# Kernel tuning notes

Measured on AMD Instinct MI355X. Metric: run time of the kernel, lower is better.

## Reference

```python
import jax, jax.numpy as jnp
import numpy as np

N_NODES = 50000
N_EDGES = 1600000
IN_FEATS = 32
HIDDEN = 64
OUT_FEAT = 64


def setup_inputs() -> dict:
    key = jax.random.key(0)
    ks = jax.random.split(key, 8)
    inputs = jax.random.normal(ks[0], (N_NODES, IN_FEATS), dtype=jnp.float32)
    edge_weights = jax.random.uniform(ks[1], (N_EDGES, 1), dtype=jnp.float32)
    src = jax.random.randint(ks[2], (N_EDGES,), 0, N_NODES, dtype=jnp.int32)
    dst = jax.random.randint(ks[3], (N_EDGES,), 0, N_NODES, dtype=jnp.int32)
    W1 = jax.random.normal(ks[4], (IN_FEATS, HIDDEN), dtype=jnp.float32) / np.sqrt(IN_FEATS)
    b1 = jnp.zeros((HIDDEN,), dtype=jnp.float32)
    W2 = jax.random.normal(ks[5], (HIDDEN + IN_FEATS, OUT_FEAT), dtype=jnp.float32) / np.sqrt(HIDDEN + IN_FEATS)
    b2 = jnp.zeros((OUT_FEAT,), dtype=jnp.float32)
    return {"inputs": inputs, "edge_weights": edge_weights, "src": src, "dst": dst,
            "W1": W1, "b1": b1, "W2": W2, "b2": b2}


def _weighted_graph_conv(x, W, b, src, dst, ew, src_norm, dst_norm, n_nodes):
    # x: [N, Din] -> [N, Dout]
    x = x @ W                               # dense projection
    x = x * src_norm                        # D_out^{-1/2} scaling at source
    m = x[src] * ew                         # [E, Dout] gather * edge weight
    h = jax.ops.segment_sum(m, dst, num_segments=n_nodes)  # scatter-sum at dest
    return h * dst_norm + b                 # D_in^{-1/2} scaling + bias


def reference(inputs, edge_weights, src, dst, W1, b1, W2, b2):
    n = inputs.shape[0]
    ones = jnp.ones((src.shape[0],), dtype=jnp.float32)
    out_deg = jax.ops.segment_sum(ones, src, num_segments=n)
    in_deg = jax.ops.segment_sum(ones, dst, num_segments=n)
    src_norm = jnp.clip(out_deg, 1.0, None)[:, None] ** -0.5  # [N,1]
    dst_norm = jnp.clip(in_deg, 1.0, None)[:, None] ** -0.5   # [N,1]

    h = _weighted_graph_conv(inputs, W1, b1, src, dst, edge_weights, src_norm, dst_norm, n)
    h = jax.nn.relu(h)
    reminder = jnp.concatenate([h, inputs], axis=-1)  # re-inject input features
    h = _weighted_graph_conv(reminder, W2, b2, src, dst, edge_weights, src_norm, dst_norm, n)
    h = jax.nn.relu(h)
    # torch F.normalize(p=2, dim=-1, eps=1e-12)
    norm = jnp.linalg.norm(h, axis=-1, keepdims=True)
    return h / jnp.maximum(norm, 1e-12)
```

## Files before the change

### kernel.cpp

```cpp
#include <hip/hip_runtime.h>
#include <math.h>


#define BUK 128
#define BUK_SHIFT 7
#define FSH 256
#define SS 128
#define HIST_BS 512
#define NBUK_MAX 512
#define MAX_LDS_BYTES 131072
#define PROJ_GRID 512

#define SCAN_BS 256
#define SCAN_ITEMS 4
#define SCAN_CHUNK (SCAN_BS * SCAN_ITEMS)

__device__ __forceinline__ unsigned short f2bf(float f) {
    unsigned u = __float_as_uint(f);
    return (unsigned short)((u + 0x7fffu + ((u >> 16) & 1u)) >> 16);
}
__device__ __forceinline__ float bf2f(unsigned short h) {
    return __uint_as_float((unsigned)h << 16);
}
__device__ __forceinline__ float rlane(float v, int k) {
    return __uint_as_float(__builtin_amdgcn_readlane(__float_as_uint(v), k));
}

__device__ __forceinline__ float edge_gather(const int* __restrict__ offsets,
                                             const unsigned* __restrict__ edata,
                                             const unsigned short* __restrict__ xp,
                                             int n, int lane) {
    int beg = offsets[n];
    int end = offsets[n + 1];
    float a0 = 0.f, a1 = 0.f, a2 = 0.f, a3 = 0.f;
    for (int p = beg; p < end; p += 64) {
        int cnt = min(64, end - p);
        unsigned eb = (p + lane < end) ? edata[p + lane] : 0u;
        int k = 0;
        for (; k + 7 < cnt; k += 8) {
            unsigned e0 = __builtin_amdgcn_readlane(eb, k);
            unsigned e1 = __builtin_amdgcn_readlane(eb, k + 1);
            unsigned e2 = __builtin_amdgcn_readlane(eb, k + 2);
            unsigned e3 = __builtin_amdgcn_readlane(eb, k + 3);
            unsigned e4 = __builtin_amdgcn_readlane(eb, k + 4);
            unsigned e5 = __builtin_amdgcn_readlane(eb, k + 5);
            unsigned e6 = __builtin_amdgcn_readlane(eb, k + 6);
            unsigned e7 = __builtin_amdgcn_readlane(eb, k + 7);
            float v0 = bf2f(xp[(size_t)(e0 & 0xffffu) * 64 + lane]);
            float v1 = bf2f(xp[(size_t)(e1 & 0xffffu) * 64 + lane]);
            float v2 = bf2f(xp[(size_t)(e2 & 0xffffu) * 64 + lane]);
            float v3 = bf2f(xp[(size_t)(e3 & 0xffffu) * 64 + lane]);
            float v4 = bf2f(xp[(size_t)(e4 & 0xffffu) * 64 + lane]);
            float v5 = bf2f(xp[(size_t)(e5 & 0xffffu) * 64 + lane]);
            float v6 = bf2f(xp[(size_t)(e6 & 0xffffu) * 64 + lane]);
            float v7 = bf2f(xp[(size_t)(e7 & 0xffffu) * 64 + lane]);
            a0 = fmaf(v0, bf2f((unsigned short)(e0 >> 16)), a0);
            a1 = fmaf(v1, bf2f((unsigned short)(e1 >> 16)), a1);
            a2 = fmaf(v2, bf2f((unsigned short)(e2 >> 16)), a2);
            a3 = fmaf(v3, bf2f((unsigned short)(e3 >> 16)), a3);
            a0 = fmaf(v4, bf2f((unsigned short)(e4 >> 16)), a0);
            a1 = fmaf(v5, bf2f((unsigned short)(e5 >> 16)), a1);
            a2 = fmaf(v6, bf2f((unsigned short)(e6 >> 16)), a2);
            a3 = fmaf(v7, bf2f((unsigned short)(e7 >> 16)), a3);
        }
        for (; k < cnt; ++k) {
            unsigned e0 = __builtin_amdgcn_readlane(eb, k);
            a0 = fmaf(bf2f(xp[(size_t)(e0 & 0xffffu) * 64 + lane]),
                      bf2f((unsigned short)(e0 >> 16)), a0);
        }
    }
    return (a0 + a1) + (a2 + a3);
}

__global__ void hist_src_kernel(const int* __restrict__ src, unsigned* __restrict__ partial_s,
                                int E, int NW4, int sliceS) {
    extern __shared__ unsigned h[];
    for (int i = threadIdx.x; i < NW4; i += blockDim.x) h[i] = 0u;
    __syncthreads();
    int s = blockIdx.x;
    int beg = s * sliceS, end = min(beg + sliceS, E);
    for (int e = beg + (int)threadIdx.x; e < end; e += blockDim.x) {
        int v = src[e];
        atomicAdd(&h[v >> 2], 1u << (8 * (v & 3)));
    }
    __syncthreads();
    unsigned* o = partial_s + (size_t)s * NW4;
    for (int i = threadIdx.x; i < NW4; i += blockDim.x) o[i] = h[i];
}

__global__ void reduce_src_kernel(const unsigned* __restrict__ partial_s,
                                  float* __restrict__ srcn, int N, int NW4) {
    int w = blockIdx.x * blockDim.x + threadIdx.x;
    if (w >= NW4) return;
    unsigned run = 0;
#pragma unroll 4
    for (int s = 0; s < SS; ++s) run += partial_s[(size_t)s * NW4 + w];
    int n0 = 4 * w;
#pragma unroll
    for (int k = 0; k < 4; ++k) {
        int n = n0 + k;
        if (n < N) srcn[n] = rsqrtf(fmaxf((float)((run >> (8 * k)) & 0xffu), 1.0f));
    }
}

__global__ void count_kernel(const int* __restrict__ dst, int* __restrict__ cntmat,
                             int E, int L, int NBUK) {
    __shared__ int c[NBUK_MAX];
    for (int i = threadIdx.x; i < NBUK; i += blockDim.x) c[i] = 0;
    __syncthreads();
    int s = blockIdx.x;
    int beg = s * L, end = min(beg + L, E);
    for (int e = beg + (int)threadIdx.x; e < end; e += blockDim.x)
        atomicAdd(&c[dst[e] >> BUK_SHIFT], 1);
    __syncthreads();
    for (int b = threadIdx.x; b < NBUK; b += blockDim.x)
        cntmat[(size_t)b * FSH + s] = c[b];
}

__global__ void scan_partial(const int* __restrict__ deg, int* __restrict__ bsum, int N) {
    __shared__ int sdata[SCAN_BS];
    int t = threadIdx.x;
    int base = blockIdx.x * SCAN_CHUNK + t * SCAN_ITEMS;
    int s = 0;
#pragma unroll
    for (int k = 0; k < SCAN_ITEMS; ++k) {
        int idx = base + k;
        s += (idx < N) ? deg[idx] : 0;
    }
    sdata[t] = s;
    __syncthreads();
    for (int off = SCAN_BS / 2; off > 0; off >>= 1) {
        if (t < off) sdata[t] += sdata[t + off];
        __syncthreads();
    }
    if (t == 0) bsum[blockIdx.x] = sdata[0];
}

__global__ void scan_bsums(int* __restrict__ bsum, int NB) {
    int carry = 0;
    for (int base = 0; base < NB; base += 64) {
        int l = base + (int)threadIdx.x;
        int v = (l < NB) ? bsum[l] : 0;
        int inc = v;
#pragma unroll
        for (int off = 1; off < 64; off <<= 1) {
            int tv = __shfl_up(inc, off, 64);
            if ((int)threadIdx.x >= off) inc += tv;
        }
        if (l < NB) bsum[l] = carry + inc - v;
        carry += __shfl(inc, 63, 64);
    }
}

__global__ void scan_final(const int* __restrict__ deg, const int* __restrict__ bsum,
                           int* __restrict__ offsets, int N) {
    __shared__ int sdata[SCAN_BS];
    int t = threadIdx.x;
    int base = blockIdx.x * SCAN_CHUNK + t * SCAN_ITEMS;
    int loc[SCAN_ITEMS];
    int s = 0;
#pragma unroll
    for (int k = 0; k < SCAN_ITEMS; ++k) {
        int idx = base + k;
        loc[k] = (idx < N) ? deg[idx] : 0;
        s += loc[k];
    }
    sdata[t] = s;
    __syncthreads();
    for (int off = 1; off < SCAN_BS; off <<= 1) {
        int v = (t >= off) ? sdata[t - off] : 0;
        __syncthreads();
        sdata[t] += v;
        __syncthreads();
    }
    int excl = sdata[t] - s + bsum[blockIdx.x];
#pragma unroll
    for (int k = 0; k < SCAN_ITEMS; ++k) {
        int idx = base + k;
        if (idx < N) {
            offsets[idx] = excl;
            if (idx == N - 1) offsets[N] = excl + loc[k];
        }
        excl += loc[k];
    }
}

__global__ void place_seg_kernel(const int* __restrict__ src, const int* __restrict__ dst,
                                 const float* __restrict__ ew, const int* __restrict__ cscan,
                                 uint2* __restrict__ inter, int E, int L, int NBUK) {
    __shared__ int cur[NBUK_MAX];
    int s = blockIdx.x;
    for (int b = threadIdx.x; b < NBUK; b += blockDim.x)
        cur[b] = cscan[(size_t)b * FSH + s];
    __syncthreads();
    int beg = s * L, end = min(beg + L, E);
    for (int e = beg + (int)threadIdx.x; e < end; e += blockDim.x) {
        int d = dst[e];
        int b = d >> BUK_SHIFT;
        int pos = atomicAdd(&cur[b], 1);
        inter[pos] = make_uint2((unsigned)src[e] | ((unsigned)f2bf(ew[e]) << 16),
                                (unsigned)(d & (BUK - 1)));
    }
}

__global__ void fill_final_kernel(const uint2* __restrict__ inter,
                                  const int* __restrict__ cscan,
                                  unsigned* __restrict__ edata, int* __restrict__ offsets,
                                  float* __restrict__ dstn, int N, int NBUK) {
    __shared__ int cnt[BUK];
    __shared__ int loff[BUK];
    int b = blockIdx.x;
    int t = threadIdx.x;
    int beg = cscan[(size_t)b * FSH];
    int end = cscan[(size_t)(b + 1) * FSH];
    if (t < BUK) cnt[t] = 0;
    __syncthreads();
    for (int p = beg + t; p < end; p += blockDim.x)
        atomicAdd(&cnt[inter[p].y], 1);
    __syncthreads();
    if (t < 64) {
        int carry = 0;
#pragma unroll
        for (int base = 0; base < BUK; base += 64) {
            int v = cnt[base + t];
            int inc = v;
#pragma unroll
            for (int off = 1; off < 64; off <<= 1) {
                int tv = __shfl_up(inc, off, 64);
                if (t >= off) inc += tv;
            }
            loff[base + t] = carry + inc - v;
            carry += __shfl(inc, 63, 64);
        }
    }
    __syncthreads();
    int node0 = b << BUK_SHIFT;
    if (t < BUK) {
        int n = node0 + t;
        if (n < N) {
            offsets[n] = beg + loff[t];
            dstn[n] = rsqrtf(fmaxf((float)cnt[t], 1.0f));
        }
    }
    if (b == NBUK - 1 && t == 0) offsets[N] = end;
    __syncthreads();
    if (t < BUK) cnt[t] = 0;
    __syncthreads();
    for (int p = beg + t; p < end; p += blockDim.x) {
        uint2 r = inter[p];
        int dl = (int)r.y;
        int rk = atomicAdd(&cnt[dl], 1);
        edata[beg + loff[dl] + rk] = r.x;
    }
}

__global__ void proj1_kernel(const float* __restrict__ X, const float* __restrict__ W1,
                             const float* __restrict__ srcn,
                             unsigned short* __restrict__ xp, int N) {
    __shared__ float w[32 * 64];
    int tid = threadIdx.x;
    {
        const float4* Wv = (const float4*)W1;
        float4* wv = (float4*)w;
        for (int i = tid; i < 512; i += 256) wv[i] = Wv[i];
    }
    __syncthreads();
    int lane = tid & 63;
    int wid = tid >> 6;
    int half = lane >> 5;
    int col = lane & 31;
    int nt = (N + 15) >> 4;
    for (int t = blockIdx.x * 4 + wid; t < nt; t += gridDim.x * 4) {
        int n0 = t << 4;
        float xv[8];
        if (n0 + 16 <= N) {
#pragma unroll
            for (int m = 0; m < 8; ++m)
                xv[m] = X[(size_t)(n0 + 2 * m + half) * 32 + col];
        } else {
#pragma unroll
            for (int m = 0; m < 8; ++m) {
                int n = n0 + 2 * m + half;
                xv[m] = (n < N) ? X[(size_t)n * 32 + col] : 0.f;
            }
        }
        float acc[16];
#pragma unroll
        for (int i = 0; i < 16; ++i) acc[i] = 0.f;
#pragma unroll 8
        for (int k = 0; k < 32; ++k) {
            float wk = w[k * 64 + lane];
#pragma unroll
            for (int m = 0; m < 8; ++m) {
                acc[2 * m]     = fmaf(rlane(xv[m], k), wk, acc[2 * m]);
                acc[2 * m + 1] = fmaf(rlane(xv[m], 32 + k), wk, acc[2 * m + 1]);
            }
        }
#pragma unroll
        for (int i = 0; i < 16; ++i) {
            int n = n0 + i;
            if (n < N) xp[(size_t)n * 64 + lane] = f2bf(acc[i] * srcn[n]);
        }
    }
}

__global__ void __launch_bounds__(256, 8)
gather_h_kernel(const int* __restrict__ offsets, const unsigned* __restrict__ edata,
                const unsigned short* __restrict__ xp, const float* __restrict__ dstn,
                const float* __restrict__ b1, unsigned short* __restrict__ hout, int N) {
    int lane = threadIdx.x & 63;
    int n = blockIdx.x * 4 + (threadIdx.x >> 6);
    if (n >= N) return;
    float acc = edge_gather(offsets, edata, xp, n, lane);
    float v = fmaxf(acc * dstn[n] + b1[lane], 0.0f);
    hout[(size_t)n * 64 + lane] = f2bf(v);
}

__global__ void proj2b_kernel(const unsigned short* __restrict__ h,
                              const float* __restrict__ X,
                              const float* __restrict__ W2, const float* __restrict__ srcn,
                              unsigned short* __restrict__ xp2, int N) {
    __shared__ float w[96 * 64];
    int tid = threadIdx.x;
    {
        const float4* Wv = (const float4*)W2;
        float4* wv = (float4*)w;
        for (int i = tid; i < 1536; i += 256) wv[i] = Wv[i];
    }
    __syncthreads();
    int lane = tid & 63;
    int wid = tid >> 6;
    int half = lane >> 5;
    int col = lane & 31;
    int nt = (N + 15) >> 4;
    for (int t = blockIdx.x * 4 + wid; t < nt; t += gridDim.x * 4) {
        int n0 = t << 4;
        float xa[8], xb[8], xc[8];
        if (n0 + 16 <= N) {
#pragma unroll
            for (int m = 0; m < 8; ++m) {
                int n = n0 + 2 * m + half;
                xa[m] = bf2f(h[(size_t)n * 64 + col]);
                xb[m] = bf2f(h[(size_t)n * 64 + 32 + col]);
                xc[m] = X[(size_t)n * 32 + col];
            }
        } else {
#pragma unroll
            for (int m = 0; m < 8; ++m) {
                int n = n0 + 2 * m + half;
                bool ok = (n < N);
                xa[m] = ok ? bf2f(h[(size_t)n * 64 + col]) : 0.f;
                xb[m] = ok ? bf2f(h[(size_t)n * 64 + 32 + col]) : 0.f;
                xc[m] = ok ? X[(size_t)n * 32 + col] : 0.f;
            }
        }
        float acc[16];
#pragma unroll
        for (int i = 0; i < 16; ++i) acc[i] = 0.f;
#pragma unroll 4
        for (int k = 0; k < 32; ++k) {
            float w0 = w[k * 64 + lane];
            float w1 = w[(32 + k) * 64 + lane];
            float w2v = w[(64 + k) * 64 + lane];
#pragma unroll
            for (int m = 0; m < 8; ++m) {
                float a0 = acc[2 * m], a1 = acc[2 * m + 1];
                a0 = fmaf(rlane(xa[m], k), w0, a0);
                a1 = fmaf(rlane(xa[m], 32 + k), w0, a1);
                a0 = fmaf(rlane(xb[m], k), w1, a0);
                a1 = fmaf(rlane(xb[m], 32 + k), w1, a1);
                a0 = fmaf(rlane(xc[m], k), w2v, a0);
                a1 = fmaf(rlane(xc[m], 32 + k), w2v, a1);
                acc[2 * m] = a0;
                acc[2 * m + 1] = a1;
            }
        }
#pragma unroll
        for (int i = 0; i < 16; ++i) {
            int n = n0 + i;
            if (n < N) xp2[(size_t)n * 64 + lane] = f2bf(acc[i] * srcn[n]);
        }
    }
}

__global__ void __launch_bounds__(256, 8)
gather_final_kernel(const int* __restrict__ offsets, const unsigned* __restrict__ edata,
                    const unsigned short* __restrict__ xp2, const float* __restrict__ dstn,
                    const float* __restrict__ b2, float* __restrict__ out, int N) {
    int lane = threadIdx.x & 63;
    int n = blockIdx.x * 4 + (threadIdx.x >> 6);
    if (n >= N) return;
    float acc = edge_gather(offsets, edata, xp2, n, lane);
    float v = fmaxf(acc * dstn[n] + b2[lane], 0.0f);
    float s = v * v;
#pragma unroll
    for (int off = 32; off >= 1; off >>= 1) s += __shfl_xor(s, off, 64);
    v = v / fmaxf(sqrtf(s), 1e-12f);
    out[(size_t)n * 64 + lane] = v;
}

__global__ void deg_kernel_i(const int* __restrict__ src, const int* __restrict__ dst,
                             int* __restrict__ degs, int* __restrict__ degd, int E) {
    int i = blockIdx.x * blockDim.x + threadIdx.x;
    if (i < E) {
        atomicAdd(&degs[src[i]], 1);
        atomicAdd(&degd[dst[i]], 1);
    }
}

__global__ void norm_kernel_i(const int* __restrict__ degs, const int* __restrict__ degd,
                              float* __restrict__ srcn, float* __restrict__ dstn, int N) {
    int i = blockIdx.x * blockDim.x + threadIdx.x;
    if (i < N) {
        srcn[i] = rsqrtf(fmaxf((float)degs[i], 1.0f));
        dstn[i] = rsqrtf(fmaxf((float)degd[i], 1.0f));
    }
}

__global__ void proj2f_kernel(const float* __restrict__ h, const float* __restrict__ X,
                              const float* __restrict__ W2, const float* __restrict__ srcn,
                              unsigned short* __restrict__ xp2, int N) {
    __shared__ float w[96 * 64];
    int tid = threadIdx.x;
    {
        const float4* Wv = (const float4*)W2;
        float4* wv = (float4*)w;
        for (int i = tid; i < 1536; i += 256) wv[i] = Wv[i];
    }
    __syncthreads();
    int lane = tid & 63;
    int wid = tid >> 6;
    int half = lane >> 5;
    int col = lane & 31;
    int nt = (N + 15) >> 4;
    for (int t = blockIdx.x * 4 + wid; t < nt; t += gridDim.x * 4) {
        int n0 = t << 4;
        float xa[8], xb[8], xc[8];
#pragma unroll
        for (int m = 0; m < 8; ++m) {
            int n = n0 + 2 * m + half;
            bool ok = (n < N);
            xa[m] = ok ? h[(size_t)n * 64 + col] : 0.f;
            xb[m] = ok ? h[(size_t)n * 64 + 32 + col] : 0.f;
            xc[m] = ok ? X[(size_t)n * 32 + col] : 0.f;
        }
        float acc[16];
#pragma unroll
        for (int i = 0; i < 16; ++i) acc[i] = 0.f;
#pragma unroll 4
        for (int k = 0; k < 32; ++k) {
            float w0 = w[k * 64 + lane];
            float w1 = w[(32 + k) * 64 + lane];
            float w2v = w[(64 + k) * 64 + lane];
#pragma unroll
            for (int m = 0; m < 8; ++m) {
                float a0 = acc[2 * m], a1 = acc[2 * m + 1];
                a0 = fmaf(rlane(xa[m], k), w0, a0);
                a1 = fmaf(rlane(xa[m], 32 + k), w0, a1);
                a0 = fmaf(rlane(xb[m], k), w1, a0);
                a1 = fmaf(rlane(xb[m], 32 + k), w1, a1);
                a0 = fmaf(rlane(xc[m], k), w2v, a0);
                a1 = fmaf(rlane(xc[m], 32 + k), w2v, a1);
                acc[2 * m] = a0;
                acc[2 * m + 1] = a1;
            }
        }
#pragma unroll
        for (int i = 0; i < 16; ++i) {
            int n = n0 + i;
            if (n < N) xp2[(size_t)n * 64 + lane] = f2bf(acc[i] * srcn[n]);
        }
    }
}

__global__ void scatter_kernel(const int* __restrict__ src, const int* __restrict__ dst,
                               const float* __restrict__ ew,
                               const unsigned short* __restrict__ xp,
                               float* __restrict__ acc, int E) {
    int total = E * 64;
    int stride = gridDim.x * blockDim.x;
    for (int i = blockIdx.x * blockDim.x + threadIdx.x; i < total; i += stride) {
        int e = i >> 6;
        int f = i & 63;
        int s = src[e];
        int d = dst[e];
        float v = bf2f(xp[(size_t)s * 64 + f]) * ew[e];
        atomicAdd(&acc[(size_t)d * 64 + f], v);
    }
}

__global__ void relu_bias_kernel(float* __restrict__ h, const float* __restrict__ dstn,
                                 const float* __restrict__ b, int N) {
    int i = blockIdx.x * blockDim.x + threadIdx.x;
    if (i < N * 64) {
        int n = i >> 6;
        int j = i & 63;
        h[i] = fmaxf(h[i] * dstn[n] + b[j], 0.0f);
    }
}

__global__ void finalize_kernel(float* __restrict__ out, const float* __restrict__ dstn,
                                const float* __restrict__ b, int N) {
    int i = blockIdx.x * blockDim.x + threadIdx.x;
    int n = i >> 6;
    int f = i & 63;
    if (n >= N) return;
    float v = fmaxf(out[(size_t)n * 64 + f] * dstn[n] + b[f], 0.0f);
    float s = v * v;
#pragma unroll
    for (int off = 32; off >= 1; off >>= 1) s += __shfl_xor(s, off, 64);
    out[(size_t)n * 64 + f] = v / fmaxf(sqrtf(s), 1e-12f);
}


extern "C" void kernel_launch(void* const* d_in, const int* in_sizes, int n_in,
                              void* d_out, int out_size, void* d_ws, size_t ws_size,
                              hipStream_t stream) {
    const float* X   = (const float*)d_in[0];
    const float* ew  = (const float*)d_in[1];
    const int*   src = (const int*)d_in[2];
    const int*   dst = (const int*)d_in[3];
    const float* W1  = (const float*)d_in[4];
    const float* b1  = (const float*)d_in[5];
    const float* W2  = (const float*)d_in[6];
    const float* b2  = (const float*)d_in[7];

    const int N = in_sizes[0] / 32;
    const int E = in_sizes[2];
    const int NW4 = (N + 3) / 4;
    const int NBUK = (N + BUK - 1) / BUK;
    const int M = NBUK * FSH;
    const int L = (E + FSH - 1) / FSH;
    const int sliceS = (E + SS - 1) / SS;
    const int NBscan = (M + SCAN_CHUNK - 1) / SCAN_CHUNK;

    float* out = (float*)d_out;
    char* wsb = (char*)d_ws;

    size_t o = 0;
    auto alloc = [&](size_t bytes) { size_t p = o; o += (bytes + 255) & ~(size_t)255; return p; };
    size_t szPS = (size_t)SS * NW4 * 4;
    size_t szIN = (size_t)E * 8;
    size_t szXP = ((size_t)N * 64 * 2 + 255) & ~(size_t)255;
    size_t szH  = (size_t)N * 64 * 2;
    size_t szI = szPS > szIN ? szPS : szIN;
    if (szXP + szH > szI) szI = szXP + szH;
    size_t offI    = alloc(szI);
    size_t offEd   = alloc((size_t)E * 4);
    size_t offXP2  = alloc((size_t)N * 64 * 2);
    size_t offCS   = alloc(((size_t)M + 1) * 4);
    size_t offSrcn = alloc((size_t)N * 4);
    size_t offDstn = alloc((size_t)N * 4);
    size_t offOff  = alloc(((size_t)N + 1) * 4);
    size_t offBsum = alloc((size_t)NBscan * 4);
    size_t need = o;

    bool ok = (ws_size >= need) && (N <= 65536) && (NBUK <= NBUK_MAX) &&
              ((size_t)NW4 * 4 <= MAX_LDS_BYTES);

    if (ok) {
        unsigned*       partial_s = (unsigned*)(wsb + offI);
        uint2*          inter     = (uint2*)(wsb + offI);
        unsigned short* xp        = (unsigned short*)(wsb + offI);
        unsigned short* hbuf      = (unsigned short*)(wsb + offI + szXP);
        unsigned*       edata     = (unsigned*)(wsb + offEd);
        unsigned short* xp2       = (unsigned short*)(wsb + offXP2);
        int*            cscan     = (int*)(wsb + offCS);
        float*          srcn      = (float*)(wsb + offSrcn);
        float*          dstn      = (float*)(wsb + offDstn);
        int*            offsets   = (int*)(wsb + offOff);
        int*            bsum      = (int*)(wsb + offBsum);

        hist_src_kernel<<<SS, HIST_BS, (size_t)NW4 * 4, stream>>>(src, partial_s, E, NW4, sliceS);
        reduce_src_kernel<<<(NW4 + 255) / 256, 256, 0, stream>>>(partial_s, srcn, N, NW4);

        count_kernel<<<FSH, HIST_BS, 0, stream>>>(dst, cscan, E, L, NBUK);
        scan_partial<<<NBscan, SCAN_BS, 0, stream>>>(cscan, bsum, M);
        scan_bsums<<<1, 64, 0, stream>>>(bsum, NBscan);
        scan_final<<<NBscan, SCAN_BS, 0, stream>>>(cscan, bsum, cscan, M);
        place_seg_kernel<<<FSH, HIST_BS, 0, stream>>>(src, dst, ew, cscan, inter, E, L, NBUK);
        fill_final_kernel<<<NBUK, 256, 0, stream>>>(inter, cscan, edata, offsets, dstn, N, NBUK);

        proj1_kernel<<<PROJ_GRID, 256, 0, stream>>>(X, W1, srcn, xp, N);
        gather_h_kernel<<<(N + 3) / 4, 256, 0, stream>>>(offsets, edata, xp, dstn, b1, hbuf, N);
        proj2b_kernel<<<PROJ_GRID, 256, 0, stream>>>(hbuf, X, W2, srcn, xp2, N);
        gather_final_kernel<<<(N + 3) / 4, 256, 0, stream>>>(offsets, edata, xp2, dstn,
                                                             b2, out, N);
    } else {
        float* ws   = (float*)d_ws;
        int*   degs = (int*)ws;
        int*   degd = (int*)(ws + N);
        float* srcn = ws + 2 * (size_t)N;
        float* dstn = ws + 3 * (size_t)N;
        unsigned short* xp = (unsigned short*)(ws + 4 * (size_t)N);

        hipMemsetAsync(degs, 0, 2 * (size_t)N * sizeof(float), stream);
        hipMemsetAsync(out, 0, (size_t)N * 64 * sizeof(float), stream);

        deg_kernel_i<<<(E + 255) / 256, 256, 0, stream>>>(src, dst, degs, degd, E);
        norm_kernel_i<<<(N + 255) / 256, 256, 0, stream>>>(degs, degd, srcn, dstn, N);

        proj1_kernel<<<PROJ_GRID, 256, 0, stream>>>(X, W1, srcn, xp, N);
        scatter_kernel<<<2048, 256, 0, stream>>>(src, dst, ew, xp, out, E);
        relu_bias_kernel<<<(N * 64 + 255) / 256, 256, 0, stream>>>(out, dstn, b1, N);

        proj2f_kernel<<<PROJ_GRID, 256, 0, stream>>>(out, X, W2, srcn, xp, N);
        hipMemsetAsync(out, 0, (size_t)N * 64 * sizeof(float), stream);
        scatter_kernel<<<2048, 256, 0, stream>>>(src, dst, ew, xp, out, E);
        finalize_kernel<<<(N * 64 + 255) / 256, 256, 0, stream>>>(out, dstn, b2, N);
    }
}
```

Measured before the change: 197.4 us.

## Gather two nodes per wavefront with packed bf16x2 feature loads

Replaces the one-node-per-wavefront edge gather with a kernel where each half-wave handles one destination node and each lane loads a packed pair of bf16 features as one 32-bit word. The aim is to halve the number of memory instructions per edge and make better use of lanes for low-degree nodes (average degree is about 32). Edge data is broadcast with shuffles rather than readlane, and the loop runs to the longer of the two nodes' edge lists, so some lanes idle when degrees differ. The final L2 normalization now reduces across 32 lanes.

```diff
diff --git a/kernel.cpp b/kernel.cpp
--- a/kernel.cpp
+++ b/kernel.cpp
@@ -22,54 +22,14 @@
 __device__ __forceinline__ float bf2f(unsigned short h) {
     return __uint_as_float((unsigned)h << 16);
 }
+__device__ __forceinline__ float bflo(unsigned u) {
+    return __uint_as_float(u << 16);
+}
+__device__ __forceinline__ float bfhi(unsigned u) {
+    return __uint_as_float(u & 0xffff0000u);
+}
 __device__ __forceinline__ float rlane(float v, int k) {
     return __uint_as_float(__builtin_amdgcn_readlane(__float_as_uint(v), k));
-}
-
-__device__ __forceinline__ float edge_gather(const int* __restrict__ offsets,
-                                             const unsigned* __restrict__ edata,
-                                             const unsigned short* __restrict__ xp,
-                                             int n, int lane) {
-    int beg = offsets[n];
-    int end = offsets[n + 1];
-    float a0 = 0.f, a1 = 0.f, a2 = 0.f, a3 = 0.f;
-    for (int p = beg; p < end; p += 64) {
-        int cnt = min(64, end - p);
-        unsigned eb = (p + lane < end) ? edata[p + lane] : 0u;
-        int k = 0;
-        for (; k + 7 < cnt; k += 8) {
-            unsigned e0 = __builtin_amdgcn_readlane(eb, k);
-            unsigned e1 = __builtin_amdgcn_readlane(eb, k + 1);
-            unsigned e2 = __builtin_amdgcn_readlane(eb, k + 2);
-            unsigned e3 = __builtin_amdgcn_readlane(eb, k + 3);
-            unsigned e4 = __builtin_amdgcn_readlane(eb, k + 4);
-            unsigned e5 = __builtin_amdgcn_readlane(eb, k + 5);
-            unsigned e6 = __builtin_amdgcn_readlane(eb, k + 6);
-            unsigned e7 = __builtin_amdgcn_readlane(eb, k + 7);
-            float v0 = bf2f(xp[(size_t)(e0 & 0xffffu) * 64 + lane]);
-            float v1 = bf2f(xp[(size_t)(e1 & 0xffffu) * 64 + lane]);
-            float v2 = bf2f(xp[(size_t)(e2 & 0xffffu) * 64 + lane]);
-            float v3 = bf2f(xp[(size_t)(e3 & 0xffffu) * 64 + lane]);
-            float v4 = bf2f(xp[(size_t)(e4 & 0xffffu) * 64 + lane]);
-            float v5 = bf2f(xp[(size_t)(e5 & 0xffffu) * 64 + lane]);
-            float v6 = bf2f(xp[(size_t)(e6 & 0xffffu) * 64 + lane]);
-            float v7 = bf2f(xp[(size_t)(e7 & 0xffffu) * 64 + lane]);
-            a0 = fmaf(v0, bf2f((unsigned short)(e0 >> 16)), a0);
-            a1 = fmaf(v1, bf2f((unsigned short)(e1 >> 16)), a1);
-            a2 = fmaf(v2, bf2f((unsigned short)(e2 >> 16)), a2);
-            a3 = fmaf(v3, bf2f((unsigned short)(e3 >> 16)), a3);
-            a0 = fmaf(v4, bf2f((unsigned short)(e4 >> 16)), a0);
-            a1 = fmaf(v5, bf2f((unsigned short)(e5 >> 16)), a1);
-            a2 = fmaf(v6, bf2f((unsigned short)(e6 >> 16)), a2);
-            a3 = fmaf(v7, bf2f((unsigned short)(e7 >> 16)), a3);
-        }
-        for (; k < cnt; ++k) {
-            unsigned e0 = __builtin_amdgcn_readlane(eb, k);
-            a0 = fmaf(bf2f(xp[(size_t)(e0 & 0xffffu) * 64 + lane]),
-                      bf2f((unsigned short)(e0 >> 16)), a0);
-        }
-    }
-    return (a0 + a1) + (a2 + a3);
 }
 
 __global__ void hist_src_kernel(const int* __restrict__ src, unsigned* __restrict__ partial_s,
@@ -304,16 +264,59 @@
     }
 }
 
-__global__ void __launch_bounds__(256, 8)
-gather_h_kernel(const int* __restrict__ offsets, const unsigned* __restrict__ edata,
-                const unsigned short* __restrict__ xp, const float* __restrict__ dstn,
-                const float* __restrict__ b1, unsigned short* __restrict__ hout, int N) {
+template <bool FINAL>
+__global__ void gather2_kernel(const int* __restrict__ offsets,
+                               const unsigned* __restrict__ edata,
+                               const unsigned short* __restrict__ xp,
+                               const float* __restrict__ dstn,
+                               const float* __restrict__ bias,
+                               void* __restrict__ outv, int N) {
+    const unsigned* xpu = (const unsigned*)xp;
     int lane = threadIdx.x & 63;
-    int n = blockIdx.x * 4 + (threadIdx.x >> 6);
-    if (n >= N) return;
-    float acc = edge_gather(offsets, edata, xp, n, lane);
-    float v = fmaxf(acc * dstn[n] + b1[lane], 0.0f);
-    hout[(size_t)n * 64 + lane] = f2bf(v);
+    int c = lane & 31;
+    int n = (blockIdx.x * 4 + (threadIdx.x >> 6)) * 2 + (lane >> 5);
+    bool valid = (n < N);
+    int beg = 0, end = 0;
+    if (valid) { beg = offsets[n]; end = offsets[n + 1]; }
+    int len = end - beg;
+    int lenA = __builtin_amdgcn_readlane(len, 0);
+    int lenB = __builtin_amdgcn_readlane(len, 32);
+    int trips = ((lenA > lenB ? lenA : lenB) + 31) >> 5;
+    float a0 = 0.f, a1 = 0.f, a2 = 0.f, a3 = 0.f;
+    for (int t = 0; t < trips; ++t) {
+        int p = beg + t * 32 + c;
+        unsigned eb = (p < end) ? edata[p] : 0u;
+#pragma unroll 8
+        for (int k = 0; k < 32; k += 2) {
+            unsigned ea = __shfl(eb, (lane & 32) + k, 64);
+            unsigned ebv = __shfl(eb, (lane & 32) + k + 1, 64);
+            unsigned pka = xpu[(size_t)(ea & 0xffffu) * 32 + c];
+            unsigned pkb = xpu[(size_t)(ebv & 0xffffu) * 32 + c];
+            float ewa = bfhi(ea);
+            float ewb = bfhi(ebv);
+            a0 = fmaf(bflo(pka), ewa, a0);
+            a1 = fmaf(bfhi(pka), ewa, a1);
+            a2 = fmaf(bflo(pkb), ewb, a2);
+            a3 = fmaf(bfhi(pkb), ewb, a3);
+        }
+    }
+    if (!valid) return;
+    float s0 = a0 + a2;
+    float s1 = a1 + a3;
+    float dn = dstn[n];
+    float2 bb = ((const float2*)bias)[c];
+    float v0 = fmaxf(s0 * dn + bb.x, 0.f);
+    float v1 = fmaxf(s1 * dn + bb.y, 0.f);
+    if (FINAL) {
+        float s = v0 * v0 + v1 * v1;
+#pragma unroll
+        for (int off = 16; off >= 1; off >>= 1) s += __shfl_xor(s, off, 64);
+        float inv = 1.0f / fmaxf(sqrtf(s), 1e-12f);
+        ((float2*)((float*)outv + (size_t)n * 64))[c] = make_float2(v0 * inv, v1 * inv);
+    } else {
+        ((unsigned*)outv)[(size_t)n * 32 + c] =
+            (unsigned)f2bf(v0) | ((unsigned)f2bf(v1) << 16);
+    }
 }
 
 __global__ void proj2b_kernel(const unsigned short* __restrict__ h,
@@ -364,15 +367,15 @@
             float w2v = w[(64 + k) * 64 + lane];
 #pragma unroll
             for (int m = 0; m < 8; ++m) {
-                float a0 = acc[2 * m], a1 = acc[2 * m + 1];
-                a0 = fmaf(rlane(xa[m], k), w0, a0);
-                a1 = fmaf(rlane(xa[m], 32 + k), w0, a1);
-                a0 = fmaf(rlane(xb[m], k), w1, a0);
-                a1 = fmaf(rlane(xb[m], 32 + k), w1, a1);
-                a0 = fmaf(rlane(xc[m], k), w2v, a0);
-                a1 = fmaf(rlane(xc[m], 32 + k), w2v, a1);
-                acc[2 * m] = a0;
-                acc[2 * m + 1] = a1;
+                float p0 = acc[2 * m], p1 = acc[2 * m + 1];
+                p0 = fmaf(rlane(xa[m], k), w0, p0);
+                p1 = fmaf(rlane(xa[m], 32 + k), w0, p1);
+                p0 = fmaf(rlane(xb[m], k), w1, p0);
+                p1 = fmaf(rlane(xb[m], 32 + k), w1, p1);
+                p0 = fmaf(rlane(xc[m], k), w2v, p0);
+                p1 = fmaf(rlane(xc[m], 32 + k), w2v, p1);
+                acc[2 * m] = p0;
+                acc[2 * m + 1] = p1;
             }
         }
 #pragma unroll
@@ -381,22 +384,6 @@
             if (n < N) xp2[(size_t)n * 64 + lane] = f2bf(acc[i] * srcn[n]);
         }
     }
-}
-
-__global__ void __launch_bounds__(256, 8)
-gather_final_kernel(const int* __restrict__ offsets, const unsigned* __restrict__ edata,
-                    const unsigned short* __restrict__ xp2, const float* __restrict__ dstn,
-                    const float* __restrict__ b2, float* __restrict__ out, int N) {
-    int lane = threadIdx.x & 63;
-    int n = blockIdx.x * 4 + (threadIdx.x >> 6);
-    if (n >= N) return;
-    float acc = edge_gather(offsets, edata, xp2, n, lane);
-    float v = fmaxf(acc * dstn[n] + b2[lane], 0.0f);
-    float s = v * v;
-#pragma unroll
-    for (int off = 32; off >= 1; off >>= 1) s += __shfl_xor(s, off, 64);
-    v = v / fmaxf(sqrtf(s), 1e-12f);
-    out[(size_t)n * 64 + lane] = v;
 }
 
 __global__ void deg_kernel_i(const int* __restrict__ src, const int* __restrict__ dst,
@@ -454,15 +441,15 @@
             float w2v = w[(64 + k) * 64 + lane];
 #pragma unroll
             for (int m = 0; m < 8; ++m) {
-                float a0 = acc[2 * m], a1 = acc[2 * m + 1];
-                a0 = fmaf(rlane(xa[m], k), w0, a0);
-                a1 = fmaf(rlane(xa[m], 32 + k), w0, a1);
-                a0 = fmaf(rlane(xb[m], k), w1, a0);
-                a1 = fmaf(rlane(xb[m], 32 + k), w1, a1);
-                a0 = fmaf(rlane(xc[m], k), w2v, a0);
-                a1 = fmaf(rlane(xc[m], 32 + k), w2v, a1);
-                acc[2 * m] = a0;
-                acc[2 * m + 1] = a1;
+                float p0 = acc[2 * m], p1 = acc[2 * m + 1];
+                p0 = fmaf(rlane(xa[m], k), w0, p0);
+                p1 = fmaf(rlane(xa[m], 32 + k), w0, p1);
+                p0 = fmaf(rlane(xb[m], k), w1, p0);
+                p1 = fmaf(rlane(xb[m], 32 + k), w1, p1);
+                p0 = fmaf(rlane(xc[m], k), w2v, p0);
+                p1 = fmaf(rlane(xc[m], 32 + k), w2v, p1);
+                acc[2 * m] = p0;
+                acc[2 * m + 1] = p1;
             }
         }
 #pragma unroll
@@ -533,6 +520,7 @@
     const int L = (E + FSH - 1) / FSH;
     const int sliceS = (E + SS - 1) / SS;
     const int NBscan = (M + SCAN_CHUNK - 1) / SCAN_CHUNK;
+    const int gatherGrid = (((N + 1) / 2) + 3) / 4;
 
     float* out = (float*)d_out;
     char* wsb = (char*)d_ws;
@@ -582,10 +570,11 @@
         fill_final_kernel<<<NBUK, 256, 0, stream>>>(inter, cscan, edata, offsets, dstn, N, NBUK);
 
         proj1_kernel<<<PROJ_GRID, 256, 0, stream>>>(X, W1, srcn, xp, N);
-        gather_h_kernel<<<(N + 3) / 4, 256, 0, stream>>>(offsets, edata, xp, dstn, b1, hbuf, N);
+        gather2_kernel<false><<<gatherGrid, 256, 0, stream>>>(offsets, edata, xp, dstn,
+                                                              b1, (void*)hbuf, N);
         proj2b_kernel<<<PROJ_GRID, 256, 0, stream>>>(hbuf, X, W2, srcn, xp2, N);
-        gather_final_kernel<<<(N + 3) / 4, 256, 0, stream>>>(offsets, edata, xp2, dstn,
-                                                             b2, out, N);
+        gather2_kernel<true><<<gatherGrid, 256, 0, stream>>>(offsets, edata, xp2, dstn,
+                                                             b2, (void*)out, N);
     } else {
         float* ws   = (float*)d_ws;
         int*   degs = (int*)ws;
```

After: 178.5 us. -9.6%, faster.
